# Kernel tuning notes

Measured on AMD Instinct MI355X. Metric: run time of the kernel, lower is better.

## Reference

```python
import jax, jax.numpy as jnp
import numpy as np

DIM = 128
N = 4096


def setup_inputs() -> dict:
    key = jax.random.key(0)
    ks = jax.random.split(key, 12)
    d = DIM
    s = 0.02
    inp = jax.random.normal(ks[0], (N, 2 * d), dtype=jnp.float32)
    # H = myLinear: (2d -> 5d -> 1), tanh after each layer
    Hw1 = jax.random.normal(ks[1], (2 * d, 5 * d), dtype=jnp.float32) * s
    Hb1 = jax.random.normal(ks[2], (5 * d,), dtype=jnp.float32) * s
    Hw2 = jax.random.normal(ks[3], (5 * d, 1), dtype=jnp.float32) * s
    Hb2 = jax.random.normal(ks[4], (1,), dtype=jnp.float32) * s
    # augment_f: (d -> 4d -> 8d -> d*d), tanh after each layer
    Aw1 = jax.random.normal(ks[5], (d, 4 * d), dtype=jnp.float32) * s
    Ab1 = jax.random.normal(ks[6], (4 * d,), dtype=jnp.float32) * s
    Aw2 = jax.random.normal(ks[7], (4 * d, 8 * d), dtype=jnp.float32) * s
    Ab2 = jax.random.normal(ks[8], (8 * d,), dtype=jnp.float32) * s
    Aw3 = jax.random.normal(ks[9], (8 * d, d * d), dtype=jnp.float32) * s
    Ab3 = jax.random.normal(ks[10], (d * d,), dtype=jnp.float32) * s
    u = jax.random.uniform(ks[11], (d,), dtype=jnp.float32, minval=-0.001, maxval=0.001)
    return {"t": 0, "inp": inp, "Hw1": Hw1, "Hb1": Hb1, "Hw2": Hw2, "Hb2": Hb2,
            "Aw1": Aw1, "Ab1": Ab1, "Aw2": Aw2, "Ab2": Ab2, "Aw3": Aw3, "Ab3": Ab3, "u": u}


def reference(t, inp, Hw1, Hb1, Hw2, Hb2, Aw1, Ab1, Aw2, Ab2, Aw3, Ab3, u):
    d = DIM
    n = inp.shape[0]

    def H_scalar(z):  # z: [2d] -> scalar
        h = jnp.tanh(z @ Hw1 + Hb1)
        return jnp.tanh(h @ Hw2 + Hb2)[0]

    # per-sample gradient of scalar H w.r.t. input (== batch_jacobian squeeze)
    g = jax.vmap(jax.grad(H_scalar))(inp)  # [N, 2d]
    dx = g[:, :d]
    dv = -g[:, d:]

    x = inp[:, :d]
    h1 = jnp.tanh(x @ Aw1 + Ab1)            # [N, 4d]
    h2 = jnp.tanh(h1 @ Aw2 + Ab2)           # [N, 8d]
    gq = jnp.tanh(h2 @ Aw3 + Ab3).reshape(n, d, d)  # [N, d, d]
    dv = dv + jnp.einsum("nij,j->ni", gq, u)
    return jnp.concatenate([dx, dv], axis=-1)  # [N, 2d]
```

## Files before the change

### kernel.cpp

```cpp
#include <hip/hip_runtime.h>
#include <hip/hip_bf16.h>
#include <cstdint>
#include <cmath>


typedef __bf16 bf16_t;
typedef __bf16 bf16x4_t __attribute__((ext_vector_type(4)));
typedef __bf16 bf16x8_t __attribute__((ext_vector_type(8)));
typedef float f32x4_t __attribute__((ext_vector_type(4)));
typedef float f32x16_t __attribute__((ext_vector_type(16)));
typedef int intx4_t __attribute__((ext_vector_type(4)));
typedef int intx8_t __attribute__((ext_vector_type(8)));

#define DIMD 128
#define NROW 4096

__device__ __forceinline__ float fast_tanh(float x) {
  float t = __builtin_amdgcn_exp2f(x * 2.8853900817779268f);
  return 1.f - 2.f * __builtin_amdgcn_rcpf(t + 1.f);
}

__device__ __forceinline__ uint8_t to_fp8(float x) {
  return (uint8_t)(__builtin_amdgcn_cvt_pk_fp8_f32(x, x, 0, false) & 0xff);
}

__device__ __forceinline__ void g2l16(const void* gp, void* lp) {
  __builtin_amdgcn_global_load_lds(
      reinterpret_cast<__attribute__((address_space(1))) void*>(
          reinterpret_cast<uintptr_t>(gp)),
      reinterpret_cast<__attribute__((address_space(3))) void*>(
          reinterpret_cast<uintptr_t>(lp)),
      16, 0, 0);
}

template <int EPI>
__global__ __launch_bounds__(256) void gemm_bt(
    const bf16_t* __restrict__ A, int lda, const bf16_t* __restrict__ B,
    int ldb, int K, const float* __restrict__ bias, void* __restrict__ outp,
    int ldo) {
  constexpr int BM = 128, BN = 128, BK = 32;
  __shared__ __align__(16) bf16_t As[BM * BK];
  __shared__ __align__(16) bf16_t Bs[BN * BK];

  const int m0 = blockIdx.x * BM;
  const int n0 = blockIdx.y * BN;
  const int tid = threadIdx.x;
  const int wave = tid >> 6;
  const int lane = tid & 63;
  const int wm = wave >> 1;
  const int wn = wave & 1;

  const int sr = lane >> 2;
  const int sk = (((lane & 3) ^ ((sr >> 1) & 3)) * 8);
  const int fr = lane & 15;
  const int fk = (((lane >> 4) ^ ((fr >> 1) & 3)) * 8);

  f32x4_t acc[4][4] = {};

  for (int k0 = 0; k0 < K; k0 += BK) {
    if (k0) __syncthreads();
#pragma unroll
    for (int t = 0; t < 2; ++t) {
      const int rb = wave * 32 + t * 16;
      g2l16(A + (size_t)(m0 + rb + sr) * lda + (k0 + sk), As + rb * BK);
      g2l16(B + (size_t)(n0 + rb + sr) * ldb + (k0 + sk), Bs + rb * BK);
    }
    __syncthreads();

    bf16x8_t af[4], bb[4];
#pragma unroll
    for (int t = 0; t < 4; ++t) {
      af[t] = *(const bf16x8_t*)(As + (wm * 64 + t * 16 + fr) * BK + fk);
      bb[t] = *(const bf16x8_t*)(Bs + (wn * 64 + t * 16 + fr) * BK + fk);
    }
#pragma unroll
    for (int i = 0; i < 4; ++i)
#pragma unroll
      for (int j = 0; j < 4; ++j)
        acc[i][j] =
            __builtin_amdgcn_mfma_f32_16x16x32_bf16(af[i], bb[j], acc[i][j], 0, 0, 0);
  }

  if constexpr (EPI == 0) {
    bf16_t* O = (bf16_t*)outp;
#pragma unroll
    for (int i = 0; i < 4; ++i) {
      const int row = m0 + wm * 64 + i * 16 + (lane >> 4) * 4;
#pragma unroll
      for (int j = 0; j < 4; ++j) {
        const int col = n0 + wn * 64 + j * 16 + fr;
        const float b = bias[col];
#pragma unroll
        for (int r = 0; r < 4; ++r)
          O[(size_t)(row + r) * ldo + col] = (bf16_t)fast_tanh(acc[i][j][r] + b);
      }
    }
  } else if constexpr (EPI == 1) {
    float* O = (float*)outp;
    const float sgn = (n0 >= DIMD) ? -1.f : 1.f;
#pragma unroll
    for (int i = 0; i < 4; ++i) {
      const int row = m0 + wm * 64 + i * 16 + (lane >> 4) * 4;
#pragma unroll
      for (int j = 0; j < 4; ++j) {
        const int col = n0 + wn * 64 + j * 16 + fr;
#pragma unroll
        for (int r = 0; r < 4; ++r)
          O[(size_t)(row + r) * ldo + col] = sgn * acc[i][j][r];
      }
    }
  } else {
    uint8_t* O = (uint8_t*)outp;
#pragma unroll
    for (int i = 0; i < 4; ++i) {
      const int row = m0 + wm * 64 + i * 16 + (lane >> 4) * 4;
#pragma unroll
      for (int j = 0; j < 4; ++j) {
        const int col = n0 + wn * 64 + j * 16 + fr;
        const float b = bias[col];
#pragma unroll
        for (int r = 0; r < 4; ++r)
          O[(size_t)(row + r) * ldo + col] =
              to_fp8(64.f * fast_tanh(acc[i][j][r] + b));
      }
    }
  }
}

__global__ __launch_bounds__(256) void gemm_a3_fp8(
    const uint8_t* __restrict__ A, const uint8_t* __restrict__ B,
    float* __restrict__ out, const float* __restrict__ ab3,
    const float* __restrict__ uvec) {
  constexpr int BK = 64, K = 1024;
  __shared__ __align__(16) uint8_t As[128 * BK];
  __shared__ __align__(16) uint8_t Bs[128 * BK];
  __shared__ float red[128], us[128], a3s[128];

  const int m0 = blockIdx.x * 128;
  const int n0 = blockIdx.y * 128;
  const int tid = threadIdx.x;
  const int wave = tid >> 6;
  const int lane = tid & 63;
  const int wm = wave >> 1;
  const int wn = wave & 1;

  if (tid < 128) {
    red[tid] = 0.f;
    us[tid] = uvec[tid];
    a3s[tid] = ab3[n0 + tid];
  }

  const int sr = lane >> 2;
  const int sk = ((lane & 3) ^ ((sr >> 1) & 3)) * 16;

  const int rl = lane & 31;
  const int w = (rl >> 1) & 3;
  const int c0 = lane >> 5;
  const int sLo = ((2 * c0) ^ w) * 16;
  const int sHi = ((2 * c0 + 1) ^ w) * 16;

  f32x16_t acc[2][2] = {};

  for (int k0 = 0; k0 < K; k0 += BK) {
    if (k0) __syncthreads();
#pragma unroll
    for (int t = 0; t < 2; ++t) {
      const int rb = t * 64 + wave * 16;
      g2l16(A + (size_t)(m0 + rb + sr) * K + (k0 + sk), As + rb * BK);
      g2l16(B + (size_t)(n0 + rb + sr) * K + (k0 + sk), Bs + rb * BK);
    }
    __syncthreads();

    intx8_t af[2], bf[2];
#pragma unroll
    for (int i = 0; i < 2; ++i) {
      const int ra = (wm * 64 + i * 32 + rl) * BK;
      intx4_t lo = *(const intx4_t*)(As + ra + sLo);
      intx4_t hi = *(const intx4_t*)(As + ra + sHi);
      af[i] = __builtin_shufflevector(lo, hi, 0, 1, 2, 3, 4, 5, 6, 7);
      const int rb = (wn * 64 + i * 32 + rl) * BK;
      intx4_t lob = *(const intx4_t*)(Bs + rb + sLo);
      intx4_t hib = *(const intx4_t*)(Bs + rb + sHi);
      bf[i] = __builtin_shufflevector(lob, hib, 0, 1, 2, 3, 4, 5, 6, 7);
    }
#pragma unroll
    for (int i = 0; i < 2; ++i)
#pragma unroll
      for (int j = 0; j < 2; ++j)
        acc[i][j] = __builtin_amdgcn_mfma_scale_f32_32x32x64_f8f6f4(
            af[i], bf[j], acc[i][j], 0 , 0 ,
            0, 0x79797979 , 0, 0x79797979 );
  }

  const int q = lane >> 5;
#pragma unroll
  for (int i = 0; i < 2; ++i) {
    float sums[16];
#pragma unroll
    for (int r = 0; r < 16; ++r) sums[r] = 0.f;
#pragma unroll
    for (int j = 0; j < 2; ++j) {
      const int c = wn * 64 + j * 32 + rl;
      const float uu = us[c];
      const float b3 = a3s[c];
#pragma unroll
      for (int r = 0; r < 16; ++r)
        sums[r] += fast_tanh(acc[i][j][r] + b3) * uu;
    }
#pragma unroll
    for (int d = 1; d < 32; d <<= 1)
#pragma unroll
      for (int r = 0; r < 16; ++r) sums[r] += __shfl_xor(sums[r], d, 64);
    if (rl == 0) {
      const int rowb = wm * 64 + i * 32 + 4 * q;
#pragma unroll
      for (int r = 0; r < 16; ++r)
        atomicAdd(&red[rowb + (r & 3) + 8 * (r >> 2)], sums[r]);
    }
  }
  __syncthreads();
  if (tid < 128) {
    const size_t idx = (size_t)(m0 + tid) * (2 * DIMD) + DIMD + blockIdx.y;
    out[idx] += red[tid];
  }
}

__global__ __launch_bounds__(256) void cvt2(const float4* __restrict__ a,
                                            bf16x4_t* __restrict__ oa, int na4,
                                            const float4* __restrict__ b,
                                            bf16x4_t* __restrict__ ob, int nb4) {
  const int i = blockIdx.x * 256 + threadIdx.x;
  const float4* in;
  bf16x4_t* out;
  int j;
  if (i < na4) {
    in = a; out = oa; j = i;
  } else {
    j = i - na4;
    if (j >= nb4) return;
    in = b; out = ob;
  }
  const float4 v = in[j];
  bf16x4_t o = {(bf16_t)v.x, (bf16_t)v.y, (bf16_t)v.z, (bf16_t)v.w};
  out[j] = o;
}

__device__ __forceinline__ void tcvt_body(const float* in, bf16_t* out, int R,
                                          int C, int bx, int by) {
  __shared__ float t[32][33];
  const int c0 = bx * 32;
  const int r0 = by * 32;
  const int tx = threadIdx.x & 31;
  const int ty = threadIdx.x >> 5;
#pragma unroll
  for (int k = 0; k < 4; ++k)
    t[ty + k * 8][tx] = in[(size_t)(r0 + ty + k * 8) * C + c0 + tx];
  __syncthreads();
#pragma unroll
  for (int k = 0; k < 4; ++k)
    out[(size_t)(c0 + ty + k * 8) * R + r0 + tx] = (bf16_t)t[tx][ty + k * 8];
}

__global__ __launch_bounds__(256) void tcvt_big_fp8(const float* __restrict__ in,
                                                    uint8_t* __restrict__ out) {
  __shared__ float t[32][33];
  const int c0 = blockIdx.x * 32;
  const int r0 = blockIdx.y * 32;
  const int tx = threadIdx.x & 31;
  const int ty = threadIdx.x >> 5;
#pragma unroll
  for (int k = 0; k < 4; ++k)
    t[ty + k * 8][tx] = in[(size_t)(r0 + ty + k * 8) * 16384 + c0 + tx];
  __syncthreads();
#pragma unroll
  for (int k = 0; k < 4; ++k)
    out[(size_t)(c0 + ty + k * 8) * 1024 + r0 + tx] =
        to_fp8(64.f * t[tx][ty + k * 8]);
}

__global__ __launch_bounds__(256) void tcvt_small(
    const float* __restrict__ Hw1, bf16_t* __restrict__ Hw1T,
    const float* __restrict__ Aw1, bf16_t* __restrict__ Aw1T,
    const float* __restrict__ Aw2, bf16_t* __restrict__ Aw2T) {
  int b = blockIdx.x;
  if (b < 160) {
    tcvt_body(Hw1, Hw1T, 256, 640, b % 20, b / 20);
  } else if (b < 224) {
    b -= 160;
    tcvt_body(Aw1, Aw1T, 128, 512, b % 16, b / 16);
  } else {
    b -= 224;
    tcvt_body(Aw2, Aw2T, 512, 1024, b % 32, b / 32);
  }
}

__global__ __launch_bounds__(64) void hgrad_w(const bf16_t* __restrict__ h,
                                              const float* __restrict__ Hw2,
                                              const float* __restrict__ Hb2,
                                              bf16_t* __restrict__ w) {
  const int row = blockIdx.x;
  const int lane = threadIdx.x;
  float hv[10], wv[10];
  float pre2 = 0.f;
#pragma unroll
  for (int t = 0; t < 10; ++t) {
    const int j = lane + t * 64;
    hv[t] = (float)h[(size_t)row * 640 + j];
    wv[t] = Hw2[j];
    pre2 += hv[t] * wv[t];
  }
#pragma unroll
  for (int d = 1; d < 64; d <<= 1) pre2 += __shfl_xor(pre2, d, 64);
  const float y = fast_tanh(pre2 + Hb2[0]);
  const float s = 1.f - y * y;
#pragma unroll
  for (int t = 0; t < 10; ++t) {
    const int j = lane + t * 64;
    w[(size_t)row * 640 + j] = (bf16_t)(s * wv[t] * (1.f - hv[t] * hv[t]));
  }
}

extern "C" void kernel_launch(void* const* d_in, const int* in_sizes, int n_in,
                              void* d_out, int out_size, void* d_ws,
                              size_t ws_size, hipStream_t stream) {
  (void)in_sizes;
  (void)n_in;
  (void)out_size;
  (void)ws_size;
  const float* inp = (const float*)d_in[1];
  const float* Hw1 = (const float*)d_in[2];
  const float* Hb1 = (const float*)d_in[3];
  const float* Hw2 = (const float*)d_in[4];
  const float* Hb2 = (const float*)d_in[5];
  const float* Aw1 = (const float*)d_in[6];
  const float* Ab1 = (const float*)d_in[7];
  const float* Aw2 = (const float*)d_in[8];
  const float* Ab2 = (const float*)d_in[9];
  const float* Aw3 = (const float*)d_in[10];
  const float* Ab3 = (const float*)d_in[11];
  const float* u = (const float*)d_in[12];
  float* out = (float*)d_out;

  char* ws = (char*)d_ws;
  bf16_t* inp_bf = (bf16_t*)ws;   ws += (size_t)NROW * 256 * 2;
  bf16_t* Hw1_bf = (bf16_t*)ws;   ws += (size_t)256 * 640 * 2;
  bf16_t* Hw1T = (bf16_t*)ws;     ws += (size_t)640 * 256 * 2;
  bf16_t* Aw1T = (bf16_t*)ws;     ws += (size_t)512 * 128 * 2;
  bf16_t* Aw2T = (bf16_t*)ws;     ws += (size_t)1024 * 512 * 2;
  uint8_t* Aw3T8 = (uint8_t*)ws;  ws += (size_t)16384 * 1024;
  bf16_t* h_bf = (bf16_t*)ws;     ws += (size_t)NROW * 640 * 2;
  bf16_t* w_bf = (bf16_t*)ws;     ws += (size_t)NROW * 640 * 2;
  bf16_t* h1_bf = (bf16_t*)ws;    ws += (size_t)NROW * 512 * 2;
  uint8_t* h2_f8 = (uint8_t*)ws;  ws += (size_t)NROW * 1024;

  const int na4 = NROW * 256 / 4, nb4 = 256 * 640 / 4;
  cvt2<<<(na4 + nb4 + 255) / 256, 256, 0, stream>>>(
      (const float4*)inp, (bf16x4_t*)inp_bf, na4, (const float4*)Hw1,
      (bf16x4_t*)Hw1_bf, nb4);
  tcvt_small<<<736, 256, 0, stream>>>(Hw1, Hw1T, Aw1, Aw1T, Aw2, Aw2T);
  tcvt_big_fp8<<<dim3(16384 / 32, 1024 / 32), 256, 0, stream>>>(Aw3, Aw3T8);

  gemm_bt<0><<<dim3(32, 5), 256, 0, stream>>>(inp_bf, 256, Hw1T, 256, 256, Hb1,
                                              h_bf, 640);
  hgrad_w<<<NROW, 64, 0, stream>>>(h_bf, Hw2, Hb2, w_bf);
  gemm_bt<1><<<dim3(32, 2), 256, 0, stream>>>(w_bf, 640, Hw1_bf, 640, 640,
                                              nullptr, out, 256);

  gemm_bt<0><<<dim3(32, 4), 256, 0, stream>>>(inp_bf, 256, Aw1T, 128, 128, Ab1,
                                              h1_bf, 512);
  gemm_bt<3><<<dim3(32, 8), 256, 0, stream>>>(h1_bf, 512, Aw2T, 512, 512, Ab2,
                                              h2_f8, 1024);
  gemm_a3_fp8<<<dim3(32, 128), 256, 0, stream>>>(h2_f8, Aw3T8, out, Ab3, u);
}
```

Baseline: 277.5 us.

## Double K-tile depth in fp8 Aw3 GEMM with new LDS layout; merge prep kernels

```diff
diff --git a/kernel.cpp b/kernel.cpp
--- a/kernel.cpp
+++ b/kernel.cpp
@@ -131,9 +131,9 @@
     const uint8_t* __restrict__ A, const uint8_t* __restrict__ B,
     float* __restrict__ out, const float* __restrict__ ab3,
     const float* __restrict__ uvec) {
-  constexpr int BK = 64, K = 1024;
-  __shared__ __align__(16) uint8_t As[128 * BK];
-  __shared__ __align__(16) uint8_t Bs[128 * BK];
+  constexpr int K = 1024, BK = 128, KS = BK / 64;
+  __shared__ __align__(16) uint8_t As[16384];
+  __shared__ __align__(16) uint8_t Bs[16384];
   __shared__ float red[128], us[128], a3s[128];
 
   const int m0 = blockIdx.x * 128;
@@ -143,6 +143,8 @@
   const int lane = tid & 63;
   const int wm = wave >> 1;
   const int wn = wave & 1;
+  const int rl = lane & 31;
+  const int c0 = lane >> 5;
 
   if (tid < 128) {
     red[tid] = 0.f;
@@ -150,46 +152,54 @@
     a3s[tid] = ab3[n0 + tid];
   }
 
-  const int sr = lane >> 2;
-  const int sk = ((lane & 3) ^ ((sr >> 1) & 3)) * 16;
-
-  const int rl = lane & 31;
-  const int w = (rl >> 1) & 3;
-  const int c0 = lane >> 5;
-  const int sLo = ((2 * c0) ^ w) * 16;
-  const int sHi = ((2 * c0 + 1) ^ w) * 16;
+  const int sb = lane >> 3;
+  const int sq = ((lane & 7) - sb) & 7;
+  const int s_rl = sb * 4 + (sq >> 1);
+  const int s_h = sq & 1;
+  const size_t aRow = (size_t)(m0 + wave * 32 + s_rl) * K + s_h * 16;
+  const size_t bRow = (size_t)(n0 + wave * 32 + s_rl) * K + s_h * 16;
+
+  const int f0 = ((((2 * (rl & 3) + (rl >> 2)) & 7) + ((rl >> 2) << 3)) << 4);
+  const int f1 =
+      ((((2 * (rl & 3) + (rl >> 2) + 1) & 7) + ((rl >> 2) << 3)) << 4);
 
   f32x16_t acc[2][2] = {};
 
   for (int k0 = 0; k0 < K; k0 += BK) {
     if (k0) __syncthreads();
 #pragma unroll
-    for (int t = 0; t < 2; ++t) {
-      const int rb = t * 64 + wave * 16;
-      g2l16(A + (size_t)(m0 + rb + sr) * K + (k0 + sk), As + rb * BK);
-      g2l16(B + (size_t)(n0 + rb + sr) * K + (k0 + sk), Bs + rb * BK);
-    }
+    for (int ks = 0; ks < KS; ++ks)
+#pragma unroll
+      for (int cc = 0; cc < 2; ++cc) {
+        const int rbase = ((ks * 4 + wave) * 2 + cc) * 1024;
+        const int gofs = k0 + ks * 64 + cc * 32;
+        g2l16(A + aRow + gofs, As + rbase);
+        g2l16(B + bRow + gofs, Bs + rbase);
+      }
     __syncthreads();
 
-    intx8_t af[2], bf[2];
-#pragma unroll
-    for (int i = 0; i < 2; ++i) {
-      const int ra = (wm * 64 + i * 32 + rl) * BK;
-      intx4_t lo = *(const intx4_t*)(As + ra + sLo);
-      intx4_t hi = *(const intx4_t*)(As + ra + sHi);
-      af[i] = __builtin_shufflevector(lo, hi, 0, 1, 2, 3, 4, 5, 6, 7);
-      const int rb = (wn * 64 + i * 32 + rl) * BK;
-      intx4_t lob = *(const intx4_t*)(Bs + rb + sLo);
-      intx4_t hib = *(const intx4_t*)(Bs + rb + sHi);
-      bf[i] = __builtin_shufflevector(lob, hib, 0, 1, 2, 3, 4, 5, 6, 7);
-    }
-#pragma unroll
-    for (int i = 0; i < 2; ++i)
-#pragma unroll
-      for (int j = 0; j < 2; ++j)
-        acc[i][j] = __builtin_amdgcn_mfma_scale_f32_32x32x64_f8f6f4(
-            af[i], bf[j], acc[i][j], 0 , 0 ,
-            0, 0x79797979 , 0, 0x79797979 );
+#pragma unroll
+    for (int ks = 0; ks < KS; ++ks) {
+      intx8_t af[2], bf[2];
+#pragma unroll
+      for (int i = 0; i < 2; ++i) {
+        const int ra = ((ks * 4 + (wm * 2 + i)) * 2 + c0) * 1024;
+        intx4_t lo = *(const intx4_t*)(As + ra + f0);
+        intx4_t hi = *(const intx4_t*)(As + ra + f1);
+        af[i] = __builtin_shufflevector(lo, hi, 0, 1, 2, 3, 4, 5, 6, 7);
+        const int rb = ((ks * 4 + (wn * 2 + i)) * 2 + c0) * 1024;
+        intx4_t lob = *(const intx4_t*)(Bs + rb + f0);
+        intx4_t hib = *(const intx4_t*)(Bs + rb + f1);
+        bf[i] = __builtin_shufflevector(lob, hib, 0, 1, 2, 3, 4, 5, 6, 7);
+      }
+#pragma unroll
+      for (int i = 0; i < 2; ++i)
+#pragma unroll
+        for (int j = 0; j < 2; ++j)
+          acc[i][j] = __builtin_amdgcn_mfma_scale_f32_32x32x64_f8f6f4(
+              af[i], bf[j], acc[i][j], 0 , 0 ,
+              0, 0x79797979 , 0, 0x79797979 );
+    }
   }
 
   const int q = lane >> 5;
@@ -223,26 +233,6 @@
     const size_t idx = (size_t)(m0 + tid) * (2 * DIMD) + DIMD + blockIdx.y;
     out[idx] += red[tid];
   }
-}
-
-__global__ __launch_bounds__(256) void cvt2(const float4* __restrict__ a,
-                                            bf16x4_t* __restrict__ oa, int na4,
-                                            const float4* __restrict__ b,
-                                            bf16x4_t* __restrict__ ob, int nb4) {
-  const int i = blockIdx.x * 256 + threadIdx.x;
-  const float4* in;
-  bf16x4_t* out;
-  int j;
-  if (i < na4) {
-    in = a; out = oa; j = i;
-  } else {
-    j = i - na4;
-    if (j >= nb4) return;
-    in = b; out = ob;
-  }
-  const float4 v = in[j];
-  bf16x4_t o = {(bf16_t)v.x, (bf16_t)v.y, (bf16_t)v.z, (bf16_t)v.w};
-  out[j] = o;
 }
 
 __device__ __forceinline__ void tcvt_body(const float* in, bf16_t* out, int R,
@@ -261,36 +251,55 @@
     out[(size_t)(c0 + ty + k * 8) * R + r0 + tx] = (bf16_t)t[tx][ty + k * 8];
 }
 
-__global__ __launch_bounds__(256) void tcvt_big_fp8(const float* __restrict__ in,
-                                                    uint8_t* __restrict__ out) {
-  __shared__ float t[32][33];
-  const int c0 = blockIdx.x * 32;
-  const int r0 = blockIdx.y * 32;
-  const int tx = threadIdx.x & 31;
-  const int ty = threadIdx.x >> 5;
-#pragma unroll
-  for (int k = 0; k < 4; ++k)
-    t[ty + k * 8][tx] = in[(size_t)(r0 + ty + k * 8) * 16384 + c0 + tx];
-  __syncthreads();
-#pragma unroll
-  for (int k = 0; k < 4; ++k)
-    out[(size_t)(c0 + ty + k * 8) * 1024 + r0 + tx] =
-        to_fp8(64.f * t[tx][ty + k * 8]);
-}
-
-__global__ __launch_bounds__(256) void tcvt_small(
-    const float* __restrict__ Hw1, bf16_t* __restrict__ Hw1T,
-    const float* __restrict__ Aw1, bf16_t* __restrict__ Aw1T,
-    const float* __restrict__ Aw2, bf16_t* __restrict__ Aw2T) {
+__global__ __launch_bounds__(256) void prep(
+    const float* __restrict__ inp, bf16_t* __restrict__ inp_bf,
+    const float* __restrict__ Hw1, bf16_t* __restrict__ Hw1_bf,
+    bf16_t* __restrict__ Hw1T, const float* __restrict__ Aw1,
+    bf16_t* __restrict__ Aw1T, const float* __restrict__ Aw2,
+    bf16_t* __restrict__ Aw2T, const float* __restrict__ Aw3,
+    uint8_t* __restrict__ Aw3T8) {
   int b = blockIdx.x;
-  if (b < 160) {
-    tcvt_body(Hw1, Hw1T, 256, 640, b % 20, b / 20);
-  } else if (b < 224) {
-    b -= 160;
-    tcvt_body(Aw1, Aw1T, 128, 512, b % 16, b / 16);
+  if (b < 16384) {
+    __shared__ float t[32][33];
+    const int c0 = (b & 511) * 32;
+    const int r0 = (b >> 9) * 32;
+    const int tx = threadIdx.x & 31;
+    const int ty = threadIdx.x >> 5;
+#pragma unroll
+    for (int k = 0; k < 4; ++k)
+      t[ty + k * 8][tx] = Aw3[(size_t)(r0 + ty + k * 8) * 16384 + c0 + tx];
+    __syncthreads();
+#pragma unroll
+    for (int k = 0; k < 4; ++k)
+      Aw3T8[(size_t)(c0 + ty + k * 8) * 1024 + r0 + tx] =
+          to_fp8(64.f * t[tx][ty + k * 8]);
+  } else if (b < 16384 + 1184) {
+    const int i = (b - 16384) * 256 + threadIdx.x;
+    const int na4 = NROW * 256 / 4;
+    const float4* in;
+    bf16x4_t* out;
+    int j;
+    if (i < na4) {
+      in = (const float4*)inp; out = (bf16x4_t*)inp_bf; j = i;
+    } else {
+      j = i - na4;
+      if (j >= 256 * 640 / 4) return;
+      in = (const float4*)Hw1; out = (bf16x4_t*)Hw1_bf;
+    }
+    const float4 v = in[j];
+    bf16x4_t o = {(bf16_t)v.x, (bf16_t)v.y, (bf16_t)v.z, (bf16_t)v.w};
+    out[j] = o;
   } else {
-    b -= 224;
-    tcvt_body(Aw2, Aw2T, 512, 1024, b % 32, b / 32);
+    int s = b - (16384 + 1184);
+    if (s < 160) {
+      tcvt_body(Hw1, Hw1T, 256, 640, s % 20, s / 20);
+    } else if (s < 224) {
+      s -= 160;
+      tcvt_body(Aw1, Aw1T, 128, 512, s % 16, s / 16);
+    } else {
+      s -= 224;
+      tcvt_body(Aw2, Aw2T, 512, 1024, s % 32, s / 32);
+    }
   }
 }
 
@@ -353,12 +362,9 @@
   bf16_t* h1_bf = (bf16_t*)ws;    ws += (size_t)NROW * 512 * 2;
   uint8_t* h2_f8 = (uint8_t*)ws;  ws += (size_t)NROW * 1024;
 
-  const int na4 = NROW * 256 / 4, nb4 = 256 * 640 / 4;
-  cvt2<<<(na4 + nb4 + 255) / 256, 256, 0, stream>>>(
-      (const float4*)inp, (bf16x4_t*)inp_bf, na4, (const float4*)Hw1,
-      (bf16x4_t*)Hw1_bf, nb4);
-  tcvt_small<<<736, 256, 0, stream>>>(Hw1, Hw1T, Aw1, Aw1T, Aw2, Aw2T);
-  tcvt_big_fp8<<<dim3(16384 / 32, 1024 / 32), 256, 0, stream>>>(Aw3, Aw3T8);
+  prep<<<16384 + 1184 + 736, 256, 0, stream>>>(inp, inp_bf, Hw1, Hw1_bf, Hw1T,
+                                               Aw1, Aw1T, Aw2, Aw2T, Aw3,
+                                               Aw3T8);
 
   gemm_bt<0><<<dim3(32, 5), 256, 0, stream>>>(inp_bf, 256, Hw1T, 256, 256, Hb1,
                                               h_bf, 640);
```

Result: no change. 277.2 us (-0.1%).

## Merge independent kernels into grouped launches and route dv through scratch

Applied to the files above, without the earlier changes.

```diff
diff --git a/kernel.cpp b/kernel.cpp
--- a/kernel.cpp
+++ b/kernel.cpp
@@ -1,7 +1,6 @@
 #include <hip/hip_runtime.h>
 #include <hip/hip_bf16.h>
 #include <cstdint>
-#include <cmath>
 
 
 typedef __bf16 bf16_t;
@@ -14,6 +13,7 @@
 
 #define DIMD 128
 #define NROW 4096
+#define SMEM_BYTES 18432
 
 __device__ __forceinline__ float fast_tanh(float x) {
   float t = __builtin_amdgcn_exp2f(x * 2.8853900817779268f);
@@ -34,16 +34,17 @@
 }
 
 template <int EPI>
-__global__ __launch_bounds__(256) void gemm_bt(
-    const bf16_t* __restrict__ A, int lda, const bf16_t* __restrict__ B,
-    int ldb, int K, const float* __restrict__ bias, void* __restrict__ outp,
-    int ldo) {
-  constexpr int BM = 128, BN = 128, BK = 32;
-  __shared__ __align__(16) bf16_t As[BM * BK];
-  __shared__ __align__(16) bf16_t Bs[BN * BK];
-
-  const int m0 = blockIdx.x * BM;
-  const int n0 = blockIdx.y * BN;
+__device__ __forceinline__ void gemm_body(char* smem, int bx, int by,
+                                          const bf16_t* A, int lda,
+                                          const bf16_t* B, int ldb, int K,
+                                          const float* bias, void* outp,
+                                          int ldo) {
+  constexpr int BK = 32;
+  bf16_t* As = (bf16_t*)smem;
+  bf16_t* Bs = As + 4096;
+
+  const int m0 = bx * 128;
+  const int n0 = by * 128;
   const int tid = threadIdx.x;
   const int wave = tid >> 6;
   const int lane = tid & 63;
@@ -77,8 +78,8 @@
     for (int i = 0; i < 4; ++i)
 #pragma unroll
       for (int j = 0; j < 4; ++j)
-        acc[i][j] =
-            __builtin_amdgcn_mfma_f32_16x16x32_bf16(af[i], bb[j], acc[i][j], 0, 0, 0);
+        acc[i][j] = __builtin_amdgcn_mfma_f32_16x16x32_bf16(af[i], bb[j],
+                                                            acc[i][j], 0, 0, 0);
   }
 
   if constexpr (EPI == 0) {
@@ -127,17 +128,19 @@
   }
 }
 
-__global__ __launch_bounds__(256) void gemm_a3_fp8(
-    const uint8_t* __restrict__ A, const uint8_t* __restrict__ B,
-    float* __restrict__ out, const float* __restrict__ ab3,
-    const float* __restrict__ uvec) {
+__device__ __forceinline__ void a3_body(char* smem, int bx, int by,
+                                        const uint8_t* A, const uint8_t* B,
+                                        float* dvA, const float* ab3,
+                                        const float* uvec) {
   constexpr int BK = 64, K = 1024;
-  __shared__ __align__(16) uint8_t As[128 * BK];
-  __shared__ __align__(16) uint8_t Bs[128 * BK];
-  __shared__ float red[128], us[128], a3s[128];
-
-  const int m0 = blockIdx.x * 128;
-  const int n0 = blockIdx.y * 128;
+  uint8_t* As = (uint8_t*)smem;
+  uint8_t* Bs = As + 8192;
+  float* red = (float*)(smem + 16384);
+  float* us = red + 128;
+  float* a3s = us + 128;
+
+  const int m0 = bx * 128;
+  const int n0 = by * 128;
   const int tid = threadIdx.x;
   const int wave = tid >> 6;
   const int lane = tid & 63;
@@ -178,9 +181,9 @@
       intx4_t lo = *(const intx4_t*)(As + ra + sLo);
       intx4_t hi = *(const intx4_t*)(As + ra + sHi);
       af[i] = __builtin_shufflevector(lo, hi, 0, 1, 2, 3, 4, 5, 6, 7);
-      const int rb = (wn * 64 + i * 32 + rl) * BK;
-      intx4_t lob = *(const intx4_t*)(Bs + rb + sLo);
-      intx4_t hib = *(const intx4_t*)(Bs + rb + sHi);
+      const int rb2 = (wn * 64 + i * 32 + rl) * BK;
+      intx4_t lob = *(const intx4_t*)(Bs + rb2 + sLo);
+      intx4_t hib = *(const intx4_t*)(Bs + rb2 + sHi);
       bf[i] = __builtin_shufflevector(lob, hib, 0, 1, 2, 3, 4, 5, 6, 7);
     }
 #pragma unroll
@@ -188,8 +191,7 @@
 #pragma unroll
       for (int j = 0; j < 2; ++j)
         acc[i][j] = __builtin_amdgcn_mfma_scale_f32_32x32x64_f8f6f4(
-            af[i], bf[j], acc[i][j], 0 , 0 ,
-            0, 0x79797979 , 0, 0x79797979 );
+            af[i], bf[j], acc[i][j], 0, 0, 0, 0x79797979, 0, 0x79797979);
   }
 
   const int q = lane >> 5;
@@ -204,8 +206,7 @@
       const float uu = us[c];
       const float b3 = a3s[c];
 #pragma unroll
-      for (int r = 0; r < 16; ++r)
-        sums[r] += fast_tanh(acc[i][j][r] + b3) * uu;
+      for (int r = 0; r < 16; ++r) sums[r] += fast_tanh(acc[i][j][r] + b3) * uu;
     }
 #pragma unroll
     for (int d = 1; d < 32; d <<= 1)
@@ -219,35 +220,13 @@
     }
   }
   __syncthreads();
-  if (tid < 128) {
-    const size_t idx = (size_t)(m0 + tid) * (2 * DIMD) + DIMD + blockIdx.y;
-    out[idx] += red[tid];
-  }
-}
-
-__global__ __launch_bounds__(256) void cvt2(const float4* __restrict__ a,
-                                            bf16x4_t* __restrict__ oa, int na4,
-                                            const float4* __restrict__ b,
-                                            bf16x4_t* __restrict__ ob, int nb4) {
-  const int i = blockIdx.x * 256 + threadIdx.x;
-  const float4* in;
-  bf16x4_t* out;
-  int j;
-  if (i < na4) {
-    in = a; out = oa; j = i;
-  } else {
-    j = i - na4;
-    if (j >= nb4) return;
-    in = b; out = ob;
-  }
-  const float4 v = in[j];
-  bf16x4_t o = {(bf16_t)v.x, (bf16_t)v.y, (bf16_t)v.z, (bf16_t)v.w};
-  out[j] = o;
-}
-
-__device__ __forceinline__ void tcvt_body(const float* in, bf16_t* out, int R,
-                                          int C, int bx, int by) {
-  __shared__ float t[32][33];
+  if (tid < 128) dvA[(size_t)(m0 + tid) * 128 + by] = red[tid];
+}
+
+__device__ __forceinline__ void tcvt_body(char* smem, const float* in,
+                                          bf16_t* out, int R, int C, int bx,
+                                          int by) {
+  float(*t)[33] = (float(*)[33])smem;
   const int c0 = bx * 32;
   const int r0 = by * 32;
   const int tx = threadIdx.x & 31;
@@ -261,45 +240,27 @@
     out[(size_t)(c0 + ty + k * 8) * R + r0 + tx] = (bf16_t)t[tx][ty + k * 8];
 }
 
-__global__ __launch_bounds__(256) void tcvt_big_fp8(const float* __restrict__ in,
-                                                    uint8_t* __restrict__ out) {
-  __shared__ float t[32][33];
-  const int c0 = blockIdx.x * 32;
-  const int r0 = blockIdx.y * 32;
+__device__ __forceinline__ void aw3t_body(char* smem, const float* Aw3,
+                                          uint8_t* Aw3T8, int b) {
+  float(*t)[33] = (float(*)[33])smem;
+  const int c0 = (b & 511) * 32;
+  const int r0 = (b >> 9) * 32;
   const int tx = threadIdx.x & 31;
   const int ty = threadIdx.x >> 5;
 #pragma unroll
   for (int k = 0; k < 4; ++k)
-    t[ty + k * 8][tx] = in[(size_t)(r0 + ty + k * 8) * 16384 + c0 + tx];
+    t[ty + k * 8][tx] = Aw3[(size_t)(r0 + ty + k * 8) * 16384 + c0 + tx];
   __syncthreads();
 #pragma unroll
   for (int k = 0; k < 4; ++k)
-    out[(size_t)(c0 + ty + k * 8) * 1024 + r0 + tx] =
+    Aw3T8[(size_t)(c0 + ty + k * 8) * 1024 + r0 + tx] =
         to_fp8(64.f * t[tx][ty + k * 8]);
 }
 
-__global__ __launch_bounds__(256) void tcvt_small(
-    const float* __restrict__ Hw1, bf16_t* __restrict__ Hw1T,
-    const float* __restrict__ Aw1, bf16_t* __restrict__ Aw1T,
-    const float* __restrict__ Aw2, bf16_t* __restrict__ Aw2T) {
-  int b = blockIdx.x;
-  if (b < 160) {
-    tcvt_body(Hw1, Hw1T, 256, 640, b % 20, b / 20);
-  } else if (b < 224) {
-    b -= 160;
-    tcvt_body(Aw1, Aw1T, 128, 512, b % 16, b / 16);
-  } else {
-    b -= 224;
-    tcvt_body(Aw2, Aw2T, 512, 1024, b % 32, b / 32);
-  }
-}
-
-__global__ __launch_bounds__(64) void hgrad_w(const bf16_t* __restrict__ h,
-                                              const float* __restrict__ Hw2,
-                                              const float* __restrict__ Hb2,
-                                              bf16_t* __restrict__ w) {
-  const int row = blockIdx.x;
-  const int lane = threadIdx.x;
+__device__ __forceinline__ void hgrad_row(int row, const bf16_t* h,
+                                          const float* Hw2, const float* Hb2,
+                                          bf16_t* wout) {
+  const int lane = threadIdx.x & 63;
   float hv[10], wv[10];
   float pre2 = 0.f;
 #pragma unroll
@@ -316,17 +277,100 @@
 #pragma unroll
   for (int t = 0; t < 10; ++t) {
     const int j = lane + t * 64;
-    w[(size_t)row * 640 + j] = (bf16_t)(s * wv[t] * (1.f - hv[t] * hv[t]));
-  }
+    wout[(size_t)row * 640 + j] = (bf16_t)(s * wv[t] * (1.f - hv[t] * hv[t]));
+  }
+}
+
+__global__ __launch_bounds__(256) void prep_small(
+    const float* __restrict__ inp, bf16_t* __restrict__ inp_bf,
+    const float* __restrict__ Hw1, bf16_t* __restrict__ Hw1_bf,
+    bf16_t* __restrict__ Hw1T, const float* __restrict__ Aw1,
+    bf16_t* __restrict__ Aw1T, const float* __restrict__ Aw2,
+    bf16_t* __restrict__ Aw2T) {
+  __shared__ __align__(16) char smem[4224];
+  int b = blockIdx.x;
+  if (b < 1184) {
+    const int i = b * 256 + threadIdx.x;
+    const int na4 = NROW * 256 / 4;
+    const float4* in;
+    bf16x4_t* out;
+    int j;
+    if (i < na4) {
+      in = (const float4*)inp; out = (bf16x4_t*)inp_bf; j = i;
+    } else {
+      j = i - na4;
+      if (j >= 256 * 640 / 4) return;
+      in = (const float4*)Hw1; out = (bf16x4_t*)Hw1_bf;
+    }
+    const float4 v = in[j];
+    bf16x4_t o = {(bf16_t)v.x, (bf16_t)v.y, (bf16_t)v.z, (bf16_t)v.w};
+    out[j] = o;
+  } else {
+    int s = b - 1184;
+    if (s < 160) tcvt_body(smem, Hw1, Hw1T, 256, 640, s % 20, s / 20);
+    else if (s < 224) { s -= 160; tcvt_body(smem, Aw1, Aw1T, 128, 512, s % 16, s / 16); }
+    else { s -= 224; tcvt_body(smem, Aw2, Aw2T, 512, 1024, s % 32, s / 32); }
+  }
+}
+
+__global__ __launch_bounds__(256) void launch1(
+    const bf16_t* __restrict__ inp_bf, const bf16_t* __restrict__ Hw1T,
+    const float* __restrict__ Hb1, bf16_t* __restrict__ h_bf,
+    const bf16_t* __restrict__ Aw1T, const float* __restrict__ Ab1,
+    bf16_t* __restrict__ h1_bf, const float* __restrict__ Aw3,
+    uint8_t* __restrict__ Aw3T8) {
+  __shared__ __align__(16) char smem[SMEM_BYTES];
+  const int b = blockIdx.x;
+  if (b < 160) {
+    gemm_body<0>(smem, b % 32, b / 32, inp_bf, 256, Hw1T, 256, 256, Hb1, h_bf, 640);
+  } else if (b < 288) {
+    const int i = b - 160;
+    gemm_body<0>(smem, i % 32, i / 32, inp_bf, 256, Aw1T, 128, 128, Ab1, h1_bf, 512);
+  } else {
+    aw3t_body(smem, Aw3, Aw3T8, b - 288);
+  }
+}
+
+__global__ __launch_bounds__(256) void launch2(
+    const bf16_t* __restrict__ h1_bf, const bf16_t* __restrict__ Aw2T,
+    const float* __restrict__ Ab2, uint8_t* __restrict__ h2_f8,
+    const bf16_t* __restrict__ h_bf, const float* __restrict__ Hw2,
+    const float* __restrict__ Hb2, bf16_t* __restrict__ w_bf) {
+  __shared__ __align__(16) char smem[SMEM_BYTES];
+  const int b = blockIdx.x;
+  if (b < 256) {
+    gemm_body<3>(smem, b % 32, b / 32, h1_bf, 512, Aw2T, 512, 512, Ab2, h2_f8, 1024);
+  } else {
+    const int row = (b - 256) * 4 + (threadIdx.x >> 6);
+    hgrad_row(row, h_bf, Hw2, Hb2, w_bf);
+  }
+}
+
+__global__ __launch_bounds__(256) void launch3(
+    const bf16_t* __restrict__ w_bf, const bf16_t* __restrict__ Hw1_bf,
+    float* __restrict__ out, const uint8_t* __restrict__ h2_f8,
+    const uint8_t* __restrict__ Aw3T8, float* __restrict__ dvA,
+    const float* __restrict__ Ab3, const float* __restrict__ uvec) {
+  __shared__ __align__(16) char smem[SMEM_BYTES];
+  const int b = blockIdx.x;
+  if (b < 64) {
+    gemm_body<1>(smem, b % 32, b / 32, w_bf, 640, Hw1_bf, 640, 640, nullptr, out, 256);
+  } else {
+    const int i = b - 64;
+    a3_body(smem, i & 31, i >> 5, h2_f8, Aw3T8, dvA, Ab3, uvec);
+  }
+}
+
+__global__ __launch_bounds__(256) void combine(float* __restrict__ out,
+                                               const float* __restrict__ dvA) {
+  const int i = blockIdx.x * 256 + threadIdx.x;
+  out[(size_t)(i >> 7) * 256 + 128 + (i & 127)] += dvA[i];
 }
 
 extern "C" void kernel_launch(void* const* d_in, const int* in_sizes, int n_in,
                               void* d_out, int out_size, void* d_ws,
                               size_t ws_size, hipStream_t stream) {
-  (void)in_sizes;
-  (void)n_in;
-  (void)out_size;
-  (void)ws_size;
+  (void)in_sizes; (void)n_in; (void)out_size; (void)ws_size;
   const float* inp = (const float*)d_in[1];
   const float* Hw1 = (const float*)d_in[2];
   const float* Hb1 = (const float*)d_in[3];
@@ -352,23 +396,15 @@
   bf16_t* w_bf = (bf16_t*)ws;     ws += (size_t)NROW * 640 * 2;
   bf16_t* h1_bf = (bf16_t*)ws;    ws += (size_t)NROW * 512 * 2;
   uint8_t* h2_f8 = (uint8_t*)ws;  ws += (size_t)NROW * 1024;
-
-  const int na4 = NROW * 256 / 4, nb4 = 256 * 640 / 4;
-  cvt2<<<(na4 + nb4 + 255) / 256, 256, 0, stream>>>(
-      (const float4*)inp, (bf16x4_t*)inp_bf, na4, (const float4*)Hw1,
-      (bf16x4_t*)Hw1_bf, nb4);
-  tcvt_small<<<736, 256, 0, stream>>>(Hw1, Hw1T, Aw1, Aw1T, Aw2, Aw2T);
-  tcvt_big_fp8<<<dim3(16384 / 32, 1024 / 32), 256, 0, stream>>>(Aw3, Aw3T8);
-
-  gemm_bt<0><<<dim3(32, 5), 256, 0, stream>>>(inp_bf, 256, Hw1T, 256, 256, Hb1,
-                                              h_bf, 640);
-  hgrad_w<<<NROW, 64, 0, stream>>>(h_bf, Hw2, Hb2, w_bf);
-  gemm_bt<1><<<dim3(32, 2), 256, 0, stream>>>(w_bf, 640, Hw1_bf, 640, 640,
-                                              nullptr, out, 256);
-
-  gemm_bt<0><<<dim3(32, 4), 256, 0, stream>>>(inp_bf, 256, Aw1T, 128, 128, Ab1,
-                                              h1_bf, 512);
-  gemm_bt<3><<<dim3(32, 8), 256, 0, stream>>>(h1_bf, 512, Aw2T, 512, 512, Ab2,
-                                              h2_f8, 1024);
-  gemm_a3_fp8<<<dim3(32, 128), 256, 0, stream>>>(h2_f8, Aw3T8, out, Ab3, u);
-}
+  float* dvA = (float*)ws;        ws += (size_t)NROW * 128 * 4;
+
+  prep_small<<<1920, 256, 0, stream>>>(inp, inp_bf, Hw1, Hw1_bf, Hw1T, Aw1,
+                                       Aw1T, Aw2, Aw2T);
+  launch1<<<288 + 16384, 256, 0, stream>>>(inp_bf, Hw1T, Hb1, h_bf, Aw1T, Ab1,
+                                           h1_bf, Aw3, Aw3T8);
+  launch2<<<256 + 1024, 256, 0, stream>>>(h1_bf, Aw2T, Ab2, h2_f8, h_bf, Hw2,
+                                          Hb2, w_bf);
+  launch3<<<64 + 4096, 256, 0, stream>>>(w_bf, Hw1_bf, out, h2_f8, Aw3T8, dvA,
+                                         Ab3, u);
+  combine<<<2048, 256, 0, stream>>>(out, dvA);
+}
```

After: 265.2 us. 1.05x faster.
